# Performance work log

Measured on AMD Instinct MI355X. Metric: run time of the kernel, lower is better.

## Reference

```python
import jax, jax.numpy as jnp
import numpy as np

B, N, K, DIN, H = 8, 5000, 16, 128, 128


def setup_inputs() -> dict:
    key = jax.random.key(0)
    ks = jax.random.split(key, 10)
    x = jax.random.normal(ks[0], (B, N, DIN), dtype=jnp.float32)
    neighbor_index = jax.random.randint(ks[1], (N, K), 0, N, dtype=jnp.int32)
    neighbor_weights = jax.random.uniform(ks[2], (N, K), dtype=jnp.float32)
    s = 1.0 / np.sqrt(H)
    W_ih = jax.random.uniform(ks[3], (4 * H, DIN), minval=-s, maxval=s, dtype=jnp.float32)
    W_hh = jax.random.uniform(ks[4], (4 * H, H), minval=-s, maxval=s, dtype=jnp.float32)
    b_ih = jax.random.uniform(ks[5], (4 * H,), minval=-s, maxval=s, dtype=jnp.float32)
    b_hh = jax.random.uniform(ks[6], (4 * H,), minval=-s, maxval=s, dtype=jnp.float32)
    W_self = jax.random.normal(ks[7], (H, DIN), dtype=jnp.float32) * 0.05
    b_self = jnp.zeros((H,), dtype=jnp.float32)
    W_comb = jax.random.normal(ks[8], (H, 2 * H), dtype=jnp.float32) * 0.05
    b_comb = jnp.zeros((H,), dtype=jnp.float32)
    return {"x": x, "neighbor_index": neighbor_index, "neighbor_weights": neighbor_weights,
            "W_ih": W_ih, "W_hh": W_hh, "b_ih": b_ih, "b_hh": b_hh,
            "W_self": W_self, "b_self": b_self, "W_comb": W_comb, "b_comb": b_comb}


def _lstm_last_h(seq, W_ih, W_hh, b_ih, b_hh):
    # seq: (M, K, DIN) -> final hidden state (M, H). PyTorch gate order: i, f, g, o.
    M = seq.shape[0]
    x_gates = jnp.einsum('mkd,gd->mkg', seq, W_ih) + b_ih  # (M, K, 4H)
    x_gates = jnp.swapaxes(x_gates, 0, 1)  # (K, M, 4H)

    def step(carry, xg):
        h, c = carry
        gates = xg + h @ W_hh.T + b_hh
        i, f, g, o = jnp.split(gates, 4, axis=-1)
        i = jax.nn.sigmoid(i); f = jax.nn.sigmoid(f); g = jnp.tanh(g); o = jax.nn.sigmoid(o)
        c = f * c + i * g
        h = o * jnp.tanh(c)
        return (h, c), None

    h0 = jnp.zeros((M, W_hh.shape[0] // 4), dtype=seq.dtype)
    (h, _), _ = jax.lax.scan(step, (h0, h0), x_gates)
    return h


def reference(x, neighbor_index, neighbor_weights, W_ih, W_hh, b_ih, b_hh, W_self, b_self, W_comb, b_comb):
    b, n, din = x.shape
    k = neighbor_index.shape[1]
    # gather neighbor feats: (B, N, K, DIN)
    neigh = jnp.take(x, neighbor_index, axis=1)
    neigh = neigh * neighbor_weights[None, :, :, None]
    lstm_in = neigh.reshape(b * n, k, din)
    agg = _lstm_last_h(lstm_in, W_ih, W_hh, b_ih, b_hh).reshape(b, n, -1)
    self_feats = x @ W_self.T + b_self
    combined = jnp.concatenate([self_feats, agg], axis=-1)
    out = jax.nn.relu(combined @ W_comb.T + b_comb)
    return out
```

## Files before the change

### kernel.cpp

```cpp
#include <hip/hip_runtime.h>
#include <math.h>

#define Bx   8
#define Nx   5000
#define Kx   16
#define DINx 128
#define Hx   128
#define G4x  512
#define Mx   40000

typedef __attribute__((ext_vector_type(8))) short sh8;
typedef __attribute__((ext_vector_type(4))) float f32x4;

__device__ __forceinline__ float sigf(float v) {
    return __fdividef(1.0f, 1.0f + __expf(-v));
}
__device__ __forceinline__ float tanf_(float v) {
    return 1.0f - __fdividef(2.0f, __expf(2.0f * v) + 1.0f);
}
__device__ __forceinline__ unsigned short rne16(float f) {
    unsigned int u = __float_as_uint(f);
    return (unsigned short)((u + 0x7fffu + ((u >> 16) & 1u)) >> 16);
}
__device__ __forceinline__ float b2f(unsigned short s) {
    return __uint_as_float(((unsigned int)s) << 16);
}

#define FMA4(P, A, Q)                                        \
    P = fmaf((A).x, (Q).x, P); P = fmaf((A).y, (Q).y, P);    \
    P = fmaf((A).z, (Q).z, P); P = fmaf((A).w, (Q).w, P);

__global__ __launch_bounds__(128) void ka(const float* __restrict__ x,
        const float* __restrict__ W_ih, const float* __restrict__ W_self,
        const float* __restrict__ b_self, float* __restrict__ G,
        float* __restrict__ S)
{
    __shared__ float xs[16 * DINx];
    const int m0 = blockIdx.x * 16;
    {
        const float4* src = (const float4*)(x + (size_t)m0 * DINx);
        float4* dst = (float4*)xs;
        #pragma unroll
        for (int i = 0; i < 4; ++i)
            dst[threadIdx.x + 128 * i] = src[threadIdx.x + 128 * i];
    }
    __syncthreads();

    const int t = threadIdx.x;
    const float4* wp[5];
    #pragma unroll
    for (int c = 0; c < 5; ++c) {
        const int o = t + 128 * c;
        wp[c] = (const float4*)((o < G4x) ? (W_ih + (size_t)o * DINx)
                                          : (W_self + (size_t)(o - G4x) * DINx));
    }
    float acc[16][5];
    #pragma unroll
    for (int n = 0; n < 16; ++n)
        #pragma unroll
        for (int c = 0; c < 5; ++c) acc[n][c] = 0.f;

    #pragma unroll 2
    for (int k4 = 0; k4 < 32; ++k4) {
        float4 wv[5];
        #pragma unroll
        for (int c = 0; c < 5; ++c) wv[c] = wp[c][k4];
        #pragma unroll
        for (int n = 0; n < 16; ++n) {
            const float4 xv = ((const float4*)(xs + n * DINx))[k4];
            #pragma unroll
            for (int c = 0; c < 5; ++c) { FMA4(acc[n][c], xv, wv[c]); }
        }
    }
    const float bs = b_self[t];
    #pragma unroll
    for (int n = 0; n < 16; ++n) {
        const size_t m = (size_t)(m0 + n);
        #pragma unroll
        for (int c = 0; c < 4; ++c)
            G[m * G4x + t + 128 * c] = acc[n][c];
        S[m * Hx + t] = acc[n][4] + bs;
    }
}

__global__ __launch_bounds__(256) void kw(const float* __restrict__ W_hh,
        const float* __restrict__ b_ih, const float* __restrict__ b_hh,
        unsigned short* __restrict__ WHp, unsigned short* __restrict__ WLp,
        float* __restrict__ bsum)
{
    const int i = blockIdx.x * 256 + threadIdx.x;
    if (i < G4x * Hx) {
        const int gdim = i >> 7, kcol = i & 127;
        const float w = W_hh[i];
        const unsigned short hi = rne16(w);
        const unsigned short lo = rne16(w - b2f(hi));
        const int dg16 = gdim >> 4, r16 = gdim & 15;
        const int kt = kcol >> 5, quad = (kcol >> 3) & 3, e = kcol & 7;
        const int pidx = (((dg16 * 4 + kt) * 64) + quad * 16 + r16) * 8 + e;
        WHp[pidx] = hi;
        WLp[pidx] = lo;
    }
    if (i < G4x) bsum[i] = b_ih[i] + b_hh[i];
}

__global__ __launch_bounds__(256, 3) void kb(const float* __restrict__ G,
        const float* __restrict__ S, const unsigned short* __restrict__ WHp,
        const unsigned short* __restrict__ WLp, const float* __restrict__ bsum,
        const int* __restrict__ nidx, const float* __restrict__ nw,
        const float* __restrict__ W_comb, const float* __restrict__ b_comb,
        float* __restrict__ out)
{
    __shared__ __align__(16) char smem[21504];
    unsigned short* hsHI = (unsigned short*)smem;
    unsigned short* hsLO = (unsigned short*)(smem + 8192);
    float*          hsF  = (float*)smem;
    int*            gofs = (int*)(smem + 17408);
    float*          wts  = (float*)(smem + 17408 + 2048);

    const int tid   = threadIdx.x;
    const int lane  = tid & 63;
    const int v     = tid >> 6;
    const int row16 = lane & 15;
    const int quad  = lane >> 4;
    const int kk    = row16 & 7;
    const int dimb  = v * 32;
    const int m0    = blockIdx.x * 32;

    for (int i = tid; i < 512; i += 256) {
        const int s = i & 31, kstep = i >> 5;
        const int m = m0 + s;
        const int bb = m / Nx;
        const int nn = m - bb * Nx;
        gofs[kstep * 32 + s] = (bb * Nx + nidx[nn * Kx + kstep]) * G4x;
        wts [kstep * 32 + s] = nw[nn * Kx + kstep];
    }
    float bsv[4][2];
    #pragma unroll
    for (int g = 0; g < 4; ++g)
        #pragma unroll
        for (int b2 = 0; b2 < 2; ++b2)
            bsv[g][b2] = bsum[g * 128 + dimb + (b2 << 4) + row16];

    float cst[2][2][4];
    #pragma unroll
    for (int mt = 0; mt < 2; ++mt)
        #pragma unroll
        for (int b2 = 0; b2 < 2; ++b2)
            #pragma unroll
            for (int j = 0; j < 4; ++j) cst[mt][b2][j] = 0.f;

    __syncthreads();

    #pragma unroll 1
    for (int k = 0; k < Kx; ++k) {
        float wkv[2][4];
        int   goff[2][4];
        #pragma unroll
        for (int mt = 0; mt < 2; ++mt)
            #pragma unroll
            for (int j = 0; j < 4; ++j) {
                const int seq = mt * 16 + quad * 4 + j;
                wkv[mt][j]  = wts[k * 32 + seq];
                goff[mt][j] = gofs[k * 32 + seq] + dimb + row16;
            }

        f32x4 acc[2][4][2];
        #pragma unroll
        for (int mt = 0; mt < 2; ++mt)
            #pragma unroll
            for (int g = 0; g < 4; ++g)
                #pragma unroll
                for (int b2 = 0; b2 < 2; ++b2)
                    #pragma unroll
                    for (int j = 0; j < 4; ++j)
                        acc[mt][g][b2][j] = fmaf(wkv[mt][j],
                            G[(size_t)(goff[mt][j] + (g << 7) + (b2 << 4))],
                            bsv[g][b2]);

        if (k) {
            #pragma unroll
            for (int kt = 0; kt < 4; ++kt) {
                const int rsw = ((kt << 2) + quad) ^ kk;
                sh8 ahi[2], alo[2];
                #pragma unroll
                for (int mt = 0; mt < 2; ++mt) {
                    const int ro = (mt * 16 + row16) * 16 + rsw;
                    ahi[mt] = ((const sh8*)hsHI)[ro];
                    alo[mt] = ((const sh8*)hsLO)[ro];
                }
                #pragma unroll
                for (int g = 0; g < 4; ++g)
                    #pragma unroll
                    for (int b2 = 0; b2 < 2; ++b2) {
                        const int wi = ((g * 8 + v * 2 + b2) * 4 + kt) * 64 + lane;
                        const sh8 wh = ((const sh8*)WHp)[wi];
                        const sh8 wl = ((const sh8*)WLp)[wi];
                        #pragma unroll
                        for (int mt = 0; mt < 2; ++mt) {
                            acc[mt][g][b2] = __builtin_amdgcn_mfma_f32_16x16x32_bf16(
                                ahi[mt], wh, acc[mt][g][b2], 0, 0, 0);
                            acc[mt][g][b2] = __builtin_amdgcn_mfma_f32_16x16x32_bf16(
                                alo[mt], wh, acc[mt][g][b2], 0, 0, 0);
                            acc[mt][g][b2] = __builtin_amdgcn_mfma_f32_16x16x32_bf16(
                                ahi[mt], wl, acc[mt][g][b2], 0, 0, 0);
                        }
                    }
            }
        }

        float hval[2][2][4];
        #pragma unroll
        for (int mt = 0; mt < 2; ++mt)
            #pragma unroll
            for (int b2 = 0; b2 < 2; ++b2)
                #pragma unroll
                for (int j = 0; j < 4; ++j) {
                    const float ig = sigf(acc[mt][0][b2][j]);
                    const float fg = sigf(acc[mt][1][b2][j]);
                    const float gg = tanf_(acc[mt][2][b2][j]);
                    const float og = sigf(acc[mt][3][b2][j]);
                    const float cc = fg * cst[mt][b2][j] + ig * gg;
                    cst[mt][b2][j] = cc;
                    hval[mt][b2][j] = og * tanf_(cc);
                }

        __syncthreads();

        if (k < Kx - 1) {
            #pragma unroll
            for (int mt = 0; mt < 2; ++mt)
                #pragma unroll
                for (int b2 = 0; b2 < 2; ++b2)
                    #pragma unroll
                    for (int j = 0; j < 4; ++j) {
                        const int seq = mt * 16 + quad * 4 + j;
                        const int dim = dimb + (b2 << 4) + row16;
                        const int idx = (seq << 7) +
                                        ((((dim >> 3) ^ (seq & 7))) << 3) + (dim & 7);
                        const float f = hval[mt][b2][j];
                        const unsigned short hi = rne16(f);
                        hsHI[idx] = hi;
                        hsLO[idx] = rne16(f - b2f(hi));
                    }
        } else {
            #pragma unroll
            for (int mt = 0; mt < 2; ++mt)
                #pragma unroll
                for (int b2 = 0; b2 < 2; ++b2)
                    #pragma unroll
                    for (int j = 0; j < 4; ++j) {
                        const int seq = mt * 16 + quad * 4 + j;
                        const int dim = dimb + (b2 << 4) + row16;
                        hsF[seq * 136 + dim] = hval[mt][b2][j];
                    }
        }
        __syncthreads();
    }

    const int dg = tid & 31;
    const int sg = tid >> 5;
    float ac[4][4];
    #pragma unroll
    for (int i = 0; i < 4; ++i)
        #pragma unroll
        for (int j = 0; j < 4; ++j) ac[i][j] = 0.f;

    const float4* S4 = (const float4*)S;
    const float4* W4 = (const float4*)W_comb;
    #pragma unroll 4
    for (int d4 = 0; d4 < 32; ++d4) {
        float4 sv[4], wv[4];
        #pragma unroll
        for (int i = 0; i < 4; ++i)
            sv[i] = S4[(size_t)(m0 + sg * 4 + i) * 32 + d4];
        #pragma unroll
        for (int j = 0; j < 4; ++j) wv[j] = W4[(dg * 4 + j) * 64 + d4];
        #pragma unroll
        for (int i = 0; i < 4; ++i) {
            #pragma unroll
            for (int j = 0; j < 4; ++j) { FMA4(ac[i][j], sv[i], wv[j]); }
        }
    }
    #pragma unroll 4
    for (int d4 = 0; d4 < 32; ++d4) {
        float4 hvv[4], wv[4];
        #pragma unroll
        for (int i = 0; i < 4; ++i)
            hvv[i] = *(const float4*)(hsF + (sg * 4 + i) * 136 + d4 * 4);
        #pragma unroll
        for (int j = 0; j < 4; ++j) wv[j] = W4[(dg * 4 + j) * 64 + 32 + d4];
        #pragma unroll
        for (int i = 0; i < 4; ++i) {
            #pragma unroll
            for (int j = 0; j < 4; ++j) { FMA4(ac[i][j], hvv[i], wv[j]); }
        }
    }
    const float4 bc = ((const float4*)b_comb)[dg];
    #pragma unroll
    for (int i = 0; i < 4; ++i) {
        float4 o4;
        o4.x = fmaxf(ac[i][0] + bc.x, 0.f);
        o4.y = fmaxf(ac[i][1] + bc.y, 0.f);
        o4.z = fmaxf(ac[i][2] + bc.z, 0.f);
        o4.w = fmaxf(ac[i][3] + bc.w, 0.f);
        *(float4*)(out + (size_t)(m0 + sg * 4 + i) * 128 + dg * 4) = o4;
    }
}

extern "C" void kernel_launch(void* const* d_in, const int* in_sizes, int n_in,
                              void* d_out, int out_size, void* d_ws, size_t ws_size,
                              hipStream_t stream)
{
    const float* x      = (const float*)d_in[0];
    const int*   nidx   = (const int*)  d_in[1];
    const float* nw     = (const float*)d_in[2];
    const float* W_ih   = (const float*)d_in[3];
    const float* W_hh   = (const float*)d_in[4];
    const float* b_ih   = (const float*)d_in[5];
    const float* b_hh   = (const float*)d_in[6];
    const float* W_self = (const float*)d_in[7];
    const float* b_self = (const float*)d_in[8];
    const float* W_comb = (const float*)d_in[9];
    const float* b_comb = (const float*)d_in[10];
    float* out = (float*)d_out;

    float* G = (float*)d_ws;
    float* S = G + (size_t)Mx * G4x;
    unsigned short* WHp = (unsigned short*)(S + (size_t)Mx * Hx);
    unsigned short* WLp = WHp + (size_t)G4x * Hx;
    float* bsum = (float*)(WLp + (size_t)G4x * Hx);

    kw<<<(G4x * Hx + 255) / 256, 256, 0, stream>>>(W_hh, b_ih, b_hh, WHp, WLp, bsum);
    ka<<<Mx / 16, 128, 0, stream>>>(x, W_ih, W_self, b_self, G, S);
    kb<<<Mx / 32, 256, 0, stream>>>(G, S, WHp, WLp, bsum, nidx, nw,
                                    W_comb, b_comb, out);
}
```

Before: 1.585 ms.

## Fuse input projection into LSTM kernel via gathered bf16x3 MFMA on x

Removes the precomputed 40000x512 fp32 gate tensor G and the scalar-FMA projection kernel. The fused kernel instead gathers neighbor x rows, stored as split bf16 hi/lo, inside the LSTM loop and computes W_ih projections with 3-pass bf16 MFMA, scaling by the neighbor weight afterwards. The self projection is also moved into the fused kernel via MFMA and staged in LDS. The aim is to cut the large G write and its scattered reads. The cost is recomputing the projection per neighbor: 16x more input-gate FLOPs than projecting each node once. It also raises LDS use and lowers occupancy to 2 blocks.

```diff
diff --git a/kernel.cpp b/kernel.cpp
--- a/kernel.cpp
+++ b/kernel.cpp
@@ -1,12 +1,9 @@
 #include <hip/hip_runtime.h>
 #include <math.h>
 
-#define Bx   8
 #define Nx   5000
 #define Kx   16
-#define DINx 128
 #define Hx   128
-#define G4x  512
 #define Mx   40000
 
 typedef __attribute__((ext_vector_type(8))) short sh8;
@@ -30,116 +27,124 @@
     P = fmaf((A).x, (Q).x, P); P = fmaf((A).y, (Q).y, P);    \
     P = fmaf((A).z, (Q).z, P); P = fmaf((A).w, (Q).w, P);
 
-__global__ __launch_bounds__(128) void ka(const float* __restrict__ x,
-        const float* __restrict__ W_ih, const float* __restrict__ W_self,
-        const float* __restrict__ b_self, float* __restrict__ G,
-        float* __restrict__ S)
-{
-    __shared__ float xs[16 * DINx];
-    const int m0 = blockIdx.x * 16;
-    {
-        const float4* src = (const float4*)(x + (size_t)m0 * DINx);
-        float4* dst = (float4*)xs;
-        #pragma unroll
-        for (int i = 0; i < 4; ++i)
-            dst[threadIdx.x + 128 * i] = src[threadIdx.x + 128 * i];
-    }
-    __syncthreads();
-
-    const int t = threadIdx.x;
-    const float4* wp[5];
-    #pragma unroll
-    for (int c = 0; c < 5; ++c) {
-        const int o = t + 128 * c;
-        wp[c] = (const float4*)((o < G4x) ? (W_ih + (size_t)o * DINx)
-                                          : (W_self + (size_t)(o - G4x) * DINx));
-    }
-    float acc[16][5];
-    #pragma unroll
-    for (int n = 0; n < 16; ++n)
-        #pragma unroll
-        for (int c = 0; c < 5; ++c) acc[n][c] = 0.f;
-
-    #pragma unroll 2
-    for (int k4 = 0; k4 < 32; ++k4) {
-        float4 wv[5];
-        #pragma unroll
-        for (int c = 0; c < 5; ++c) wv[c] = wp[c][k4];
-        #pragma unroll
-        for (int n = 0; n < 16; ++n) {
-            const float4 xv = ((const float4*)(xs + n * DINx))[k4];
-            #pragma unroll
-            for (int c = 0; c < 5; ++c) { FMA4(acc[n][c], xv, wv[c]); }
-        }
-    }
-    const float bs = b_self[t];
-    #pragma unroll
-    for (int n = 0; n < 16; ++n) {
-        const size_t m = (size_t)(m0 + n);
-        #pragma unroll
-        for (int c = 0; c < 4; ++c)
-            G[m * G4x + t + 128 * c] = acc[n][c];
-        S[m * Hx + t] = acc[n][4] + bs;
-    }
-}
-
-__global__ __launch_bounds__(256) void kw(const float* __restrict__ W_hh,
-        const float* __restrict__ b_ih, const float* __restrict__ b_hh,
-        unsigned short* __restrict__ WHp, unsigned short* __restrict__ WLp,
+#define MFMA3(ACC, XH, XL, WH, WL)                                             \
+    ACC = __builtin_amdgcn_mfma_f32_16x16x32_bf16(XH, WH, ACC, 0, 0, 0);       \
+    ACC = __builtin_amdgcn_mfma_f32_16x16x32_bf16(XL, WH, ACC, 0, 0, 0);       \
+    ACC = __builtin_amdgcn_mfma_f32_16x16x32_bf16(XH, WL, ACC, 0, 0, 0);
+
+__global__ __launch_bounds__(256) void kp(const float* __restrict__ x,
+        const float* __restrict__ W_ih, const float* __restrict__ W_hh,
+        const float* __restrict__ W_self, const float* __restrict__ b_ih,
+        const float* __restrict__ b_hh,
+        unsigned short* __restrict__ xhi, unsigned short* __restrict__ xlo,
+        unsigned short* __restrict__ WIH, unsigned short* __restrict__ WIL,
+        unsigned short* __restrict__ WHH, unsigned short* __restrict__ WHL,
+        unsigned short* __restrict__ WSH, unsigned short* __restrict__ WSL,
         float* __restrict__ bsum)
 {
     const int i = blockIdx.x * 256 + threadIdx.x;
-    if (i < G4x * Hx) {
+    if (i < Mx * 128) {
+        const float v = x[i];
+        const unsigned short h = rne16(v);
+        xhi[i] = h;
+        xlo[i] = rne16(v - b2f(h));
+    }
+    if (i < 512 * 128) {
         const int gdim = i >> 7, kcol = i & 127;
-        const float w = W_hh[i];
-        const unsigned short hi = rne16(w);
-        const unsigned short lo = rne16(w - b2f(hi));
         const int dg16 = gdim >> 4, r16 = gdim & 15;
         const int kt = kcol >> 5, quad = (kcol >> 3) & 3, e = kcol & 7;
         const int pidx = (((dg16 * 4 + kt) * 64) + quad * 16 + r16) * 8 + e;
-        WHp[pidx] = hi;
-        WLp[pidx] = lo;
-    }
-    if (i < G4x) bsum[i] = b_ih[i] + b_hh[i];
-}
-
-__global__ __launch_bounds__(256, 3) void kb(const float* __restrict__ G,
-        const float* __restrict__ S, const unsigned short* __restrict__ WHp,
-        const unsigned short* __restrict__ WLp, const float* __restrict__ bsum,
+        const float wi_ = W_ih[i];
+        const unsigned short h1 = rne16(wi_);
+        WIH[pidx] = h1; WIL[pidx] = rne16(wi_ - b2f(h1));
+        const float wh_ = W_hh[i];
+        const unsigned short h2 = rne16(wh_);
+        WHH[pidx] = h2; WHL[pidx] = rne16(wh_ - b2f(h2));
+        if (i < 128 * 128) {
+            const float ws_ = W_self[i];
+            const unsigned short h3 = rne16(ws_);
+            WSH[pidx] = h3; WSL[pidx] = rne16(ws_ - b2f(h3));
+        }
+        if (i < 512) bsum[i] = b_ih[i] + b_hh[i];
+    }
+}
+
+__global__ __launch_bounds__(256, 2) void kf(
+        const unsigned short* __restrict__ xhi, const unsigned short* __restrict__ xlo,
+        const unsigned short* __restrict__ WIH, const unsigned short* __restrict__ WIL,
+        const unsigned short* __restrict__ WHH, const unsigned short* __restrict__ WHL,
+        const unsigned short* __restrict__ WSH, const unsigned short* __restrict__ WSL,
+        const float* __restrict__ bsum, const float* __restrict__ b_self,
         const int* __restrict__ nidx, const float* __restrict__ nw,
         const float* __restrict__ W_comb, const float* __restrict__ b_comb,
         float* __restrict__ out)
 {
-    __shared__ __align__(16) char smem[21504];
+    __shared__ __align__(16) char smem[37888];
     unsigned short* hsHI = (unsigned short*)smem;
     unsigned short* hsLO = (unsigned short*)(smem + 8192);
     float*          hsF  = (float*)smem;
-    int*            gofs = (int*)(smem + 17408);
-    float*          wts  = (float*)(smem + 17408 + 2048);
-
-    const int tid   = threadIdx.x;
-    const int lane  = tid & 63;
-    const int v     = tid >> 6;
-    const int row16 = lane & 15;
-    const int quad  = lane >> 4;
-    const int kk    = row16 & 7;
-    const int dimb  = v * 32;
-    const int m0    = blockIdx.x * 32;
+    int*            gofs = (int*)(smem + 16384);
+    float*          wts  = (float*)(smem + 18432);
+    float*          hsS  = (float*)(smem + 20480);
+
+    const int tid  = threadIdx.x;
+    const int lane = tid & 63;
+    const int v    = tid >> 6;
+    const int r16  = lane & 15;
+    const int quad = lane >> 4;
+    const int kk   = r16 & 7;
+    const int dimb = v * 32;
+    const int m0   = blockIdx.x * 32;
 
     for (int i = tid; i < 512; i += 256) {
         const int s = i & 31, kstep = i >> 5;
         const int m = m0 + s;
         const int bb = m / Nx;
         const int nn = m - bb * Nx;
-        gofs[kstep * 32 + s] = (bb * Nx + nidx[nn * Kx + kstep]) * G4x;
+        gofs[kstep * 32 + s] = (bb * Nx + nidx[nn * Kx + kstep]) * 128;
         wts [kstep * 32 + s] = nw[nn * Kx + kstep];
     }
+
     float bsv[4][2];
     #pragma unroll
     for (int g = 0; g < 4; ++g)
         #pragma unroll
         for (int b2 = 0; b2 < 2; ++b2)
-            bsv[g][b2] = bsum[g * 128 + dimb + (b2 << 4) + row16];
+            bsv[g][b2] = bsum[g * 128 + dimb + (b2 << 4) + r16];
+
+    {
+        f32x4 accs[2][2];
+        const float bS0 = b_self[dimb + r16];
+        const float bS1 = b_self[dimb + 16 + r16];
+        accs[0][0] = (f32x4)bS0; accs[0][1] = (f32x4)bS1;
+        accs[1][0] = (f32x4)bS0; accs[1][1] = (f32x4)bS1;
+        #pragma unroll
+        for (int kt = 0; kt < 4; ++kt) {
+            sh8 axh[2], axl[2];
+            #pragma unroll
+            for (int mt = 0; mt < 2; ++mt) {
+                const int xe = (m0 + mt * 16 + r16) * 128 + kt * 32 + quad * 8;
+                axh[mt] = *(const sh8*)(xhi + xe);
+                axl[mt] = *(const sh8*)(xlo + xe);
+            }
+            #pragma unroll
+            for (int b2 = 0; b2 < 2; ++b2) {
+                const int wi = ((v * 2 + b2) * 4 + kt) * 64 + lane;
+                const sh8 wh = ((const sh8*)WSH)[wi];
+                const sh8 wl = ((const sh8*)WSL)[wi];
+                #pragma unroll
+                for (int mt = 0; mt < 2; ++mt) { MFMA3(accs[mt][b2], axh[mt], axl[mt], wh, wl); }
+            }
+        }
+        #pragma unroll
+        for (int mt = 0; mt < 2; ++mt)
+            #pragma unroll
+            for (int b2 = 0; b2 < 2; ++b2)
+                #pragma unroll
+                for (int j = 0; j < 4; ++j)
+                    hsS[(mt * 16 + quad * 4 + j) * 136 + dimb + (b2 << 4) + r16]
+                        = accs[mt][b2][j];
+    }
 
     float cst[2][2][4];
     #pragma unroll
@@ -153,16 +158,22 @@
 
     #pragma unroll 1
     for (int k = 0; k < Kx; ++k) {
+        sh8 gxh[2][4], gxl[2][4];
+        #pragma unroll
+        for (int mt = 0; mt < 2; ++mt) {
+            const int ro = gofs[k * 32 + mt * 16 + r16];
+            #pragma unroll
+            for (int kt = 0; kt < 4; ++kt) {
+                gxh[mt][kt] = *(const sh8*)(xhi + ro + kt * 32 + quad * 8);
+                gxl[mt][kt] = *(const sh8*)(xlo + ro + kt * 32 + quad * 8);
+            }
+        }
         float wkv[2][4];
-        int   goff[2][4];
         #pragma unroll
         for (int mt = 0; mt < 2; ++mt)
             #pragma unroll
-            for (int j = 0; j < 4; ++j) {
-                const int seq = mt * 16 + quad * 4 + j;
-                wkv[mt][j]  = wts[k * 32 + seq];
-                goff[mt][j] = gofs[k * 32 + seq] + dimb + row16;
-            }
+            for (int j = 0; j < 4; ++j)
+                wkv[mt][j] = wts[k * 32 + mt * 16 + quad * 4 + j];
 
         f32x4 acc[2][4][2];
         #pragma unroll
@@ -171,11 +182,7 @@
             for (int g = 0; g < 4; ++g)
                 #pragma unroll
                 for (int b2 = 0; b2 < 2; ++b2)
-                    #pragma unroll
-                    for (int j = 0; j < 4; ++j)
-                        acc[mt][g][b2][j] = fmaf(wkv[mt][j],
-                            G[(size_t)(goff[mt][j] + (g << 7) + (b2 << 4))],
-                            bsv[g][b2]);
+                    acc[mt][g][b2] = (f32x4)bsv[g][b2];
 
         if (k) {
             #pragma unroll
@@ -184,7 +191,7 @@
                 sh8 ahi[2], alo[2];
                 #pragma unroll
                 for (int mt = 0; mt < 2; ++mt) {
-                    const int ro = (mt * 16 + row16) * 16 + rsw;
+                    const int ro = (mt * 16 + r16) * 16 + rsw;
                     ahi[mt] = ((const sh8*)hsHI)[ro];
                     alo[mt] = ((const sh8*)hsLO)[ro];
                 }
@@ -193,19 +200,45 @@
                     #pragma unroll
                     for (int b2 = 0; b2 < 2; ++b2) {
                         const int wi = ((g * 8 + v * 2 + b2) * 4 + kt) * 64 + lane;
-                        const sh8 wh = ((const sh8*)WHp)[wi];
-                        const sh8 wl = ((const sh8*)WLp)[wi];
+                        const sh8 wh = ((const sh8*)WHH)[wi];
+                        const sh8 wl = ((const sh8*)WHL)[wi];
                         #pragma unroll
-                        for (int mt = 0; mt < 2; ++mt) {
-                            acc[mt][g][b2] = __builtin_amdgcn_mfma_f32_16x16x32_bf16(
-                                ahi[mt], wh, acc[mt][g][b2], 0, 0, 0);
-                            acc[mt][g][b2] = __builtin_amdgcn_mfma_f32_16x16x32_bf16(
-                                alo[mt], wh, acc[mt][g][b2], 0, 0, 0);
-                            acc[mt][g][b2] = __builtin_amdgcn_mfma_f32_16x16x32_bf16(
-                                ahi[mt], wl, acc[mt][g][b2], 0, 0, 0);
-                        }
+                        for (int mt = 0; mt < 2; ++mt) { MFMA3(acc[mt][g][b2], ahi[mt], alo[mt], wh, wl); }
                     }
             }
+        }
+
+        #pragma unroll
+        for (int gh = 0; gh < 2; ++gh) {
+            f32x4 a2[2][2][2];
+            #pragma unroll
+            for (int mt = 0; mt < 2; ++mt)
+                #pragma unroll
+                for (int gg = 0; gg < 2; ++gg)
+                    #pragma unroll
+                    for (int b2 = 0; b2 < 2; ++b2) a2[mt][gg][b2] = (f32x4)0.f;
+            #pragma unroll
+            for (int kt = 0; kt < 4; ++kt)
+                #pragma unroll
+                for (int gg = 0; gg < 2; ++gg)
+                    #pragma unroll
+                    for (int b2 = 0; b2 < 2; ++b2) {
+                        const int g = gh * 2 + gg;
+                        const int wi = ((g * 8 + v * 2 + b2) * 4 + kt) * 64 + lane;
+                        const sh8 wh = ((const sh8*)WIH)[wi];
+                        const sh8 wl = ((const sh8*)WIL)[wi];
+                        #pragma unroll
+                        for (int mt = 0; mt < 2; ++mt) { MFMA3(a2[mt][gg][b2], gxh[mt][kt], gxl[mt][kt], wh, wl); }
+                    }
+            #pragma unroll
+            for (int mt = 0; mt < 2; ++mt)
+                #pragma unroll
+                for (int gg = 0; gg < 2; ++gg)
+                    #pragma unroll
+                    for (int b2 = 0; b2 < 2; ++b2)
+                        #pragma unroll
+                        for (int j = 0; j < 4; ++j)
+                            acc[mt][gh * 2 + gg][b2][j] += wkv[mt][j] * a2[mt][gg][b2][j];
         }
 
         float hval[2][2][4];
@@ -234,7 +267,7 @@
                     #pragma unroll
                     for (int j = 0; j < 4; ++j) {
                         const int seq = mt * 16 + quad * 4 + j;
-                        const int dim = dimb + (b2 << 4) + row16;
+                        const int dim = dimb + (b2 << 4) + r16;
                         const int idx = (seq << 7) +
                                         ((((dim >> 3) ^ (seq & 7))) << 3) + (dim & 7);
                         const float f = hval[mt][b2][j];
@@ -250,7 +283,7 @@
                     #pragma unroll
                     for (int j = 0; j < 4; ++j) {
                         const int seq = mt * 16 + quad * 4 + j;
-                        const int dim = dimb + (b2 << 4) + row16;
+                        const int dim = dimb + (b2 << 4) + r16;
                         hsF[seq * 136 + dim] = hval[mt][b2][j];
                     }
         }
@@ -265,14 +298,13 @@
         #pragma unroll
         for (int j = 0; j < 4; ++j) ac[i][j] = 0.f;
 
-    const float4* S4 = (const float4*)S;
     const float4* W4 = (const float4*)W_comb;
     #pragma unroll 4
     for (int d4 = 0; d4 < 32; ++d4) {
         float4 sv[4], wv[4];
         #pragma unroll
         for (int i = 0; i < 4; ++i)
-            sv[i] = S4[(size_t)(m0 + sg * 4 + i) * 32 + d4];
+            sv[i] = *(const float4*)(hsS + (sg * 4 + i) * 136 + d4 * 4);
         #pragma unroll
         for (int j = 0; j < 4; ++j) wv[j] = W4[(dg * 4 + j) * 64 + d4];
         #pragma unroll
@@ -324,14 +356,18 @@
     const float* b_comb = (const float*)d_in[10];
     float* out = (float*)d_out;
 
-    float* G = (float*)d_ws;
-    float* S = G + (size_t)Mx * G4x;
-    unsigned short* WHp = (unsigned short*)(S + (size_t)Mx * Hx);
-    unsigned short* WLp = WHp + (size_t)G4x * Hx;
-    float* bsum = (float*)(WLp + (size_t)G4x * Hx);
-
-    kw<<<(G4x * Hx + 255) / 256, 256, 0, stream>>>(W_hh, b_ih, b_hh, WHp, WLp, bsum);
-    ka<<<Mx / 16, 128, 0, stream>>>(x, W_ih, W_self, b_self, G, S);
-    kb<<<Mx / 32, 256, 0, stream>>>(G, S, WHp, WLp, bsum, nidx, nw,
-                                    W_comb, b_comb, out);
-}
+    unsigned short* xhi = (unsigned short*)d_ws;
+    unsigned short* xlo = xhi + (size_t)Mx * 128;
+    unsigned short* WIH = xlo + (size_t)Mx * 128;
+    unsigned short* WIL = WIH + 512 * 128;
+    unsigned short* WHH = WIL + 512 * 128;
+    unsigned short* WHL = WHH + 512 * 128;
+    unsigned short* WSH = WHL + 512 * 128;
+    unsigned short* WSL = WSH + 128 * 128;
+    float* bsum = (float*)(WSL + 128 * 128);
+
+    kp<<<(Mx * 128 + 255) / 256, 256, 0, stream>>>(x, W_ih, W_hh, W_self,
+        b_ih, b_hh, xhi, xlo, WIH, WIL, WHH, WHL, WSH, WSL, bsum);
+    kf<<<Mx / 32, 256, 0, stream>>>(xhi, xlo, WIH, WIL, WHH, WHL, WSH, WSL,
+        bsum, b_self, nidx, nw, W_comb, b_comb, out);
+}
```

Measured after the change: 2.491 ms. 57.2% more time.
